# Performance work log

Measured on AMD Instinct MI355X. Metric: run time of the kernel, lower is better.

The kernel has to match this reference:

```python
import jax, jax.numpy as jnp
import numpy as np

GAMMA = 0.00390625  # 1/256


def setup_inputs() -> dict:
    key = jax.random.key(0)
    ks = jax.random.split(key, 8)
    B, F, S = 65536, 256, 1024
    return {
        "x": jax.random.normal(ks[0], (B, F), dtype=jnp.float32),
        "sv": jax.random.normal(ks[1], (S, F), dtype=jnp.float32),
        "W1": jax.random.normal(ks[2], (S, S), dtype=jnp.float32) * (1.0 / np.sqrt(S)),
        "b1": jax.random.normal(ks[3], (S,), dtype=jnp.float32) * 0.01,
        "W2": jax.random.normal(ks[4], (S, S), dtype=jnp.float32) * (1.0 / np.sqrt(S)),
        "b2": jax.random.normal(ks[5], (S,), dtype=jnp.float32) * 0.01,
        "Wh": jax.random.normal(ks[6], (2, S), dtype=jnp.float32) * (1.0 / np.sqrt(S)),
        "bh": jax.random.normal(ks[7], (2,), dtype=jnp.float32) * 0.01,
    }


def reference(x, sv, W1, b1, W2, b2, Wh, bh):
    # RBF kernel features: k[b, s] = exp(-gamma * ||x_b - sv_s||^2)
    # Expand squared distance to avoid a (B, S, F) intermediate.
    x2 = jnp.sum(x * x, axis=-1, keepdims=True)          # (B, 1)
    s2 = jnp.sum(sv * sv, axis=-1)[None, :]              # (1, S)
    d2 = x2 + s2 - 2.0 * jnp.einsum("bf,sf->bs", x, sv)  # (B, S)
    k = jnp.exp(-GAMMA * d2)                              # (B, S)
    # MLP classifier: depth=2 hidden ReLU layers + 2-logit head
    h = jax.nn.relu(jnp.einsum("bs,os->bo", k, W1) + b1)
    h = jax.nn.relu(jnp.einsum("bs,os->bo", h, W2) + b2)
    return jnp.einsum("bs,os->bo", h, Wh) + bh           # (B, 2)
```

## Files before the change

kernel.cpp:

```cpp
#include <hip/hip_runtime.h>

typedef _Float16 f16x8 __attribute__((ext_vector_type(8)));
typedef _Float16 f16x4 __attribute__((ext_vector_type(4)));
typedef float    f32x4 __attribute__((ext_vector_type(4)));

#define GAMMA_F 0.00390625f

__global__ __launch_bounds__(256) void prep_rows_kernel(
    const float* __restrict__ src, _Float16* __restrict__ dst,
    float* __restrict__ sq, int nrows)
{
    int lane = threadIdx.x & 63, w = threadIdx.x >> 6;
    int row = blockIdx.x * 4 + w;
    if (row >= nrows) return;
    float4 v = ((const float4*)(src + (size_t)row * 256))[lane];
    f16x4 h;
    h[0] = (_Float16)v.x; h[1] = (_Float16)v.y;
    h[2] = (_Float16)v.z; h[3] = (_Float16)v.w;
    *((f16x4*)(dst + (size_t)row * 256) + lane) = h;
    float ss = v.x*v.x + v.y*v.y + v.z*v.z + v.w*v.w;
#pragma unroll
    for (int off = 32; off; off >>= 1) ss += __shfl_down(ss, off);
    if (lane == 0) sq[row] = ss;
}

__global__ __launch_bounds__(256) void cvt_kernel(
    const float* __restrict__ src, _Float16* __restrict__ dst, int n4)
{
    int i = blockIdx.x * 256 + threadIdx.x;
    if (i < n4) {
        float4 v = ((const float4*)src)[i];
        f16x4 h;
        h[0] = (_Float16)v.x; h[1] = (_Float16)v.y;
        h[2] = (_Float16)v.z; h[3] = (_Float16)v.w;
        ((f16x4*)dst)[i] = h;
    }
}

#define SBAR()   __builtin_amdgcn_s_barrier()
#define RFENCE() asm volatile("" ::: "memory")

#define GLDA(gptr, uoff)                                                       \
    asm volatile("s_mov_b32 m0, %1\n\t"                                        \
                 "global_load_lds_dwordx4 %0, off\n\t"                         \
                 "s_mov_b32 m0, -1"                                            \
                 :: "v"((const void*)(gptr)), "s"(uoff))

#define UOF(x) __builtin_amdgcn_readfirstlane((x) + wb)

#define STA(s, h) do {                                                         \
    GLDA(aP##h##0, UOF((s)*32768 + (h)*16384));                                \
    GLDA(aP##h##1, UOF((s)*32768 + (h)*16384 + 8192));                         \
} while (0)
#define STB(s, h) do {                                                         \
    GLDA(bP##h##0, UOF(65536 + (s)*32768 + (h)*16384));                        \
    GLDA(bP##h##1, UOF(65536 + (s)*32768 + (h)*16384 + 8192));                 \
} while (0)
#define ADV_A() do { aP00+=64; aP01+=64; aP10+=64; aP11+=64; } while (0)
#define ADV_B() do { bP00+=64; bP01+=64; bP10+=64; bP11+=64; } while (0)

#define RD_A0(s, mh) do { _Pragma("unroll") for (int mi = 0; mi < 4; ++mi)     \
    a0f[mi] = *(const f16x8*)(ldsb + aO0 + (s)*32768 + (mh)*8192 + mi*2048);   \
} while (0)
#define RD_A1(s, mh) do { _Pragma("unroll") for (int mi = 0; mi < 4; ++mi)     \
    a1f[mi] = *(const f16x8*)(ldsb + aO1 + (s)*32768 + (mh)*8192 + mi*2048);   \
} while (0)
#define RD_B0A(s, nh) do { _Pragma("unroll") for (int nb = 0; nb < 2; ++nb)    \
    bA0[nb] = *(const f16x8*)(ldsb + bO0 + (s)*32768 + (nh)*4096 + nb*2048);   \
} while (0)
#define RD_B1A(s, nh) do { _Pragma("unroll") for (int nb = 0; nb < 2; ++nb)    \
    bA1[nb] = *(const f16x8*)(ldsb + bO1 + (s)*32768 + (nh)*4096 + nb*2048);   \
} while (0)
#define RD_B0B(s, nh) do { _Pragma("unroll") for (int nb = 0; nb < 2; ++nb)    \
    bB0[nb] = *(const f16x8*)(ldsb + bO0 + (s)*32768 + (nh)*4096 + nb*2048);   \
} while (0)
#define RD_B1B(s, nh) do { _Pragma("unroll") for (int nb = 0; nb < 2; ++nb)    \
    bB1[nb] = *(const f16x8*)(ldsb + bO1 + (s)*32768 + (nh)*4096 + nb*2048);   \
} while (0)

#define MFMA8(af, bf, mh, nh) do {                                             \
    _Pragma("unroll") for (int mi = 0; mi < 4; ++mi)                           \
    _Pragma("unroll") for (int nb = 0; nb < 2; ++nb)                           \
        acc[(mh)*4+mi][(nh)*2+nb] = __builtin_amdgcn_mfma_f32_16x16x32_f16(    \
            af[mi], bf[nb], acc[(mh)*4+mi][(nh)*2+nb], 0, 0, 0);               \
} while (0)

#define MFMA32(mh) do {                                                        \
    __builtin_amdgcn_s_setprio(1);                                             \
    MFMA8(a0f, bA0, mh, 0); MFMA8(a1f, bA1, mh, 0);                            \
    MFMA8(a0f, bB0, mh, 1); MFMA8(a1f, bB1, mh, 1);                            \
    __builtin_amdgcn_s_setprio(0);                                             \
} while (0)

template <int MODE, int K>
__global__ __launch_bounds__(512, 1) void gemm256_kernel(
    const _Float16* __restrict__ A, const _Float16* __restrict__ B,
    _Float16* __restrict__ C, const float* __restrict__ e0,
    const float* __restrict__ e1)
{
    constexpr int KT = K / 64;
    constexpr int NITER = KT / 2;
    __shared__ f16x8 lds[8192];
    char* ldsb = (char*)lds;

    const int t    = threadIdx.x;
    const int lane = t & 63, w = t >> 6;
    const int wb   = w << 10;
    const int wr   = w >> 2, wc = w & 3;
    const int lrow = lane & 15, kq = lane >> 4;

    int poison = 0;
    asm volatile("" : "+v"(poison));
    if (poison) lds[0] = f16x8{};

    int bid  = blockIdx.x;
    int cpx  = (int)(gridDim.x >> 3);
    int lbid = (bid & 7) * cpx + (bid >> 3);
    int bm   = lbid >> 2, bn = lbid & 3;
    int rowA0 = bm * 256, rowB0 = bn * 256;

    const int aO0 = ((wr*128 + lrow)*8 + ( kq      ^ (lrow & 7))) * 16;
    const int aO1 = ((wr*128 + lrow)*8 + ((4 + kq) ^ (lrow & 7))) * 16;
    const int bO0 = 65536 + ((wc*64 + lrow)*8 + ( kq      ^ (lrow & 7))) * 16;
    const int bO1 = 65536 + ((wc*64 + lrow)*8 + ((4 + kq) ^ (lrow & 7))) * 16;

    const int prow = t >> 3;
    const int cg   = (t & 7) ^ (prow & 7);
    const _Float16* aP00 = A + (size_t)(rowA0 + prow      ) * K + cg * 8;
    const _Float16* aP01 = aP00 + (size_t) 64 * K;
    const _Float16* aP10 = aP00 + (size_t)128 * K;
    const _Float16* aP11 = aP00 + (size_t)192 * K;
    const _Float16* bP00 = B + (size_t)(rowB0 + prow      ) * K + cg * 8;
    const _Float16* bP01 = bP00 + (size_t) 64 * K;
    const _Float16* bP10 = bP00 + (size_t)128 * K;
    const _Float16* bP11 = bP00 + (size_t)192 * K;

    f32x4 acc[8][4];
#pragma unroll
    for (int i = 0; i < 8; ++i)
#pragma unroll
        for (int j = 0; j < 4; ++j) acc[i][j] = (f32x4){0.f, 0.f, 0.f, 0.f};

    f16x8 a0f[4], a1f[4], bA0[2], bA1[2], bB0[2], bB1[2];

    STA(0,0); STA(0,1); STB(0,0); STB(0,1); ADV_A(); ADV_B();
    STA(1,0); STA(1,1); STB(1,0); STB(1,1); ADV_A(); ADV_B();
    asm volatile("s_waitcnt vmcnt(8)" ::: "memory");
    SBAR();

    for (int j = 0; j < NITER; ++j) {
        const bool last = (j == NITER - 1);

        RFENCE();
        RD_A0(0, 0); RD_B0A(0, 0); RD_B0B(0, 1);
        if (j > 0) { STA(1, 0); STA(1, 1); ADV_A(); }
        SBAR();
        RD_A1(0, 0); RD_B1A(0, 0); RD_B1B(0, 1);
        MFMA32(0);
        RFENCE();
        RD_A0(0, 1);
        if (!last) {
            STB(0, 0); STB(0, 1); ADV_B();
            asm volatile("s_waitcnt vmcnt(4)" ::: "memory");
        } else {
            asm volatile("s_waitcnt vmcnt(0)" ::: "memory");
        }
        SBAR();
        RD_A1(0, 1);
        MFMA32(1);
        RFENCE();
        RD_A0(1, 0); RD_B0A(1, 0); RD_B0B(1, 1);
        if (!last) { STA(0, 0); STA(0, 1); ADV_A(); }
        SBAR();
        RD_A1(1, 0); RD_B1A(1, 0); RD_B1B(1, 1);
        MFMA32(0);
        RFENCE();
        RD_A0(1, 1);
        if (!last) {
            STB(1, 0); STB(1, 1); ADV_B();
            asm volatile("s_waitcnt vmcnt(4)" ::: "memory");
        }
        SBAR();
        RD_A1(1, 1);
        MFMA32(1);
    }

    int gr0 = rowA0 + wr * 128;
    int gc0 = rowB0 + wc * 64;
    float ecol[4];
#pragma unroll
    for (int ni = 0; ni < 4; ++ni)
        ecol[ni] = (MODE == 0) ? e1[gc0 + ni * 16 + lrow]
                               : e0[gc0 + ni * 16 + lrow];
#pragma unroll
    for (int mi = 0; mi < 8; ++mi) {
#pragma unroll
        for (int jj = 0; jj < 4; ++jj) {
            int row = gr0 + mi * 16 + kq * 4 + jj;
            float xr = (MODE == 0) ? e0[row] : 0.f;
            size_t base = (size_t)row * 1024 + gc0 + lrow;
#pragma unroll
            for (int ni = 0; ni < 4; ++ni) {
                float v = acc[mi][ni][jj];
                if (MODE == 0) {
                    v = __expf(-GAMMA_F * (xr + ecol[ni] - 2.f * v));
                } else {
                    v += ecol[ni];
                    v = fmaxf(v, 0.f);
                }
                C[base + (size_t)ni * 16] = (_Float16)v;
            }
        }
    }
}

__global__ __launch_bounds__(256) void head_kernel(
    const _Float16* __restrict__ h2, const float* __restrict__ Wh,
    const float* __restrict__ bh, float* __restrict__ out)
{
    int lane = threadIdx.x & 63, w = threadIdx.x >> 6;
    int row = blockIdx.x * 4 + w;
    const _Float16* hp = h2 + (size_t)row * 1024;
    float s0 = 0.f, s1 = 0.f;
#pragma unroll
    for (int i = 0; i < 2; ++i) {
        int base = (i * 64 + lane) * 8;
        f16x8 hv = *(const f16x8*)(hp + base);
#pragma unroll
        for (int j = 0; j < 8; ++j) {
            float hj = (float)hv[j];
            s0 = fmaf(hj, Wh[base + j], s0);
            s1 = fmaf(hj, Wh[1024 + base + j], s1);
        }
    }
#pragma unroll
    for (int off = 32; off; off >>= 1) {
        s0 += __shfl_down(s0, off);
        s1 += __shfl_down(s1, off);
    }
    if (lane == 0) {
        out[(size_t)row * 2 + 0] = s0 + bh[0];
        out[(size_t)row * 2 + 1] = s1 + bh[1];
    }
}

extern "C" void kernel_launch(void* const* d_in, const int* in_sizes, int n_in,
                              void* d_out, int out_size, void* d_ws, size_t ws_size,
                              hipStream_t stream)
{
    const float* x  = (const float*)d_in[0];
    const float* sv = (const float*)d_in[1];
    const float* W1 = (const float*)d_in[2];
    const float* b1 = (const float*)d_in[3];
    const float* W2 = (const float*)d_in[4];
    const float* b2 = (const float*)d_in[5];
    const float* Wh = (const float*)d_in[6];
    const float* bh = (const float*)d_in[7];
    float* out = (float*)d_out;
    char* ws = (char*)d_ws;

    constexpr size_t OFF_SV = 0;
    constexpr size_t OFF_W1 = OFF_SV + 524288;
    constexpr size_t OFF_W2 = OFF_W1 + 2097152;
    constexpr size_t OFF_S2 = OFF_W2 + 2097152;
    constexpr size_t PERSIST = OFF_S2 + 4096;

    _Float16* svf = (_Float16*)(ws + OFF_SV);
    _Float16* w1f = (_Float16*)(ws + OFF_W1);
    _Float16* w2f = (_Float16*)(ws + OFF_W2);
    float*    s2v = (float*)(ws + OFF_S2);

    int Bc = 65536;
    while (Bc > 256 && PERSIST + (size_t)Bc * 4100ULL > ws_size) Bc >>= 1;

    char* chunk_base = ws + PERSIST;
    _Float16* kb  = (_Float16*)chunk_base;
    _Float16* h1b = (_Float16*)(chunk_base + (size_t)Bc * 2048);
    _Float16* xf  = h1b;
    float*    x2v = (float*)(chunk_base + (size_t)Bc * 4096);

    prep_rows_kernel<<<1024 / 4, 256, 0, stream>>>(sv, svf, s2v, 1024);
    cvt_kernel<<<1024, 256, 0, stream>>>(W1, w1f, 262144);
    cvt_kernel<<<1024, 256, 0, stream>>>(W2, w2f, 262144);

    int nchunks = 65536 / Bc;
    int ggrid   = (Bc / 256) * 4;
    for (int c = 0; c < nchunks; ++c) {
        const float* xc = x + (size_t)c * Bc * 256;
        prep_rows_kernel<<<Bc / 4, 256, 0, stream>>>(xc, xf, x2v, Bc);
        gemm256_kernel<0, 256><<<ggrid, 512, 0, stream>>>(xf, svf, kb, x2v, s2v);
        gemm256_kernel<1, 1024><<<ggrid, 512, 0, stream>>>(kb, w1f, h1b, b1, nullptr);
        gemm256_kernel<1, 1024><<<ggrid, 512, 0, stream>>>(h1b, w2f, kb, b2, nullptr);
        head_kernel<<<Bc / 4, 256, 0, stream>>>(kb, Wh, bh, out + (size_t)c * Bc * 2);
    }
}
```

Baseline: 372.7 us.

## Simplify GEMM main loop to one-barrier-per-tile double-buffered schedule

Replaces the hand-interleaved half-tile ping-pong schedule with a plain double-buffered loop. Each phase now waits for all outstanding global-to-LDS loads and hits one barrier, then reads every A/B fragment for the tile into registers. It then issues the next tile's loads into the other buffer and runs all 64 MFMAs. This removes several barriers and partial vmcnt waits per tile. In exchange it holds many more fragment registers and uses a full vmcnt(0) wait, which may expose memory latency that the finer interleaving used to hide.

```diff
diff --git a/kernel.cpp b/kernel.cpp
--- a/kernel.cpp
+++ b/kernel.cpp
@@ -38,7 +38,6 @@
 }
 
 #define SBAR()   __builtin_amdgcn_s_barrier()
-#define RFENCE() asm volatile("" ::: "memory")
 
 #define GLDA(gptr, uoff)                                                       \
     asm volatile("s_mov_b32 m0, %1\n\t"                                        \
@@ -48,48 +47,52 @@
 
 #define UOF(x) __builtin_amdgcn_readfirstlane((x) + wb)
 
-#define STA(s, h) do {                                                         \
-    GLDA(aP##h##0, UOF((s)*32768 + (h)*16384));                                \
-    GLDA(aP##h##1, UOF((s)*32768 + (h)*16384 + 8192));                         \
-} while (0)
-#define STB(s, h) do {                                                         \
-    GLDA(bP##h##0, UOF(65536 + (s)*32768 + (h)*16384));                        \
-    GLDA(bP##h##1, UOF(65536 + (s)*32768 + (h)*16384 + 8192));                 \
+#define STAGE_A(so) do {                                                       \
+    GLDA(aP00, UOF((so)*32768));                                               \
+    GLDA(aP01, UOF((so)*32768 + 8192));                                        \
+    GLDA(aP10, UOF((so)*32768 + 16384));                                       \
+    GLDA(aP11, UOF((so)*32768 + 24576));                                       \
+} while (0)
+#define STAGE_B(so) do {                                                       \
+    GLDA(bP00, UOF(65536 + (so)*32768));                                       \
+    GLDA(bP01, UOF(65536 + (so)*32768 + 8192));                                \
+    GLDA(bP10, UOF(65536 + (so)*32768 + 16384));                               \
+    GLDA(bP11, UOF(65536 + (so)*32768 + 24576));                               \
 } while (0)
 #define ADV_A() do { aP00+=64; aP01+=64; aP10+=64; aP11+=64; } while (0)
 #define ADV_B() do { bP00+=64; bP01+=64; bP10+=64; bP11+=64; } while (0)
 
-#define RD_A0(s, mh) do { _Pragma("unroll") for (int mi = 0; mi < 4; ++mi)     \
-    a0f[mi] = *(const f16x8*)(ldsb + aO0 + (s)*32768 + (mh)*8192 + mi*2048);   \
-} while (0)
-#define RD_A1(s, mh) do { _Pragma("unroll") for (int mi = 0; mi < 4; ++mi)     \
-    a1f[mi] = *(const f16x8*)(ldsb + aO1 + (s)*32768 + (mh)*8192 + mi*2048);   \
-} while (0)
-#define RD_B0A(s, nh) do { _Pragma("unroll") for (int nb = 0; nb < 2; ++nb)    \
-    bA0[nb] = *(const f16x8*)(ldsb + bO0 + (s)*32768 + (nh)*4096 + nb*2048);   \
-} while (0)
-#define RD_B1A(s, nh) do { _Pragma("unroll") for (int nb = 0; nb < 2; ++nb)    \
-    bA1[nb] = *(const f16x8*)(ldsb + bO1 + (s)*32768 + (nh)*4096 + nb*2048);   \
-} while (0)
-#define RD_B0B(s, nh) do { _Pragma("unroll") for (int nb = 0; nb < 2; ++nb)    \
-    bB0[nb] = *(const f16x8*)(ldsb + bO0 + (s)*32768 + (nh)*4096 + nb*2048);   \
-} while (0)
-#define RD_B1B(s, nh) do { _Pragma("unroll") for (int nb = 0; nb < 2; ++nb)    \
-    bB1[nb] = *(const f16x8*)(ldsb + bO1 + (s)*32768 + (nh)*4096 + nb*2048);   \
-} while (0)
-
-#define MFMA8(af, bf, mh, nh) do {                                             \
+#define RD_ALL(s) do {                                                         \
+    _Pragma("unroll") for (int mh = 0; mh < 2; ++mh)                           \
+    _Pragma("unroll") for (int mi = 0; mi < 4; ++mi) {                         \
+        af[0][mh*4+mi] = *(const f16x8*)(ldsb + aO0 + (s)*32768 + mh*8192 + mi*2048); \
+        af[1][mh*4+mi] = *(const f16x8*)(ldsb + aO1 + (s)*32768 + mh*8192 + mi*2048); \
+    }                                                                          \
+    _Pragma("unroll") for (int nh = 0; nh < 2; ++nh)                           \
+    _Pragma("unroll") for (int nb = 0; nb < 2; ++nb) {                         \
+        bf[0][nh*2+nb] = *(const f16x8*)(ldsb + bO0 + (s)*32768 + nh*4096 + nb*2048); \
+        bf[1][nh*2+nb] = *(const f16x8*)(ldsb + bO1 + (s)*32768 + nh*4096 + nb*2048); \
+    }                                                                          \
+} while (0)
+
+#define MFMA64() do {                                                          \
+    __builtin_amdgcn_s_setprio(1);                                             \
+    _Pragma("unroll") for (int ks = 0; ks < 2; ++ks)                           \
+    _Pragma("unroll") for (int mh = 0; mh < 2; ++mh)                           \
     _Pragma("unroll") for (int mi = 0; mi < 4; ++mi)                           \
+    _Pragma("unroll") for (int nh = 0; nh < 2; ++nh)                           \
     _Pragma("unroll") for (int nb = 0; nb < 2; ++nb)                           \
-        acc[(mh)*4+mi][(nh)*2+nb] = __builtin_amdgcn_mfma_f32_16x16x32_f16(    \
-            af[mi], bf[nb], acc[(mh)*4+mi][(nh)*2+nb], 0, 0, 0);               \
-} while (0)
-
-#define MFMA32(mh) do {                                                        \
-    __builtin_amdgcn_s_setprio(1);                                             \
-    MFMA8(a0f, bA0, mh, 0); MFMA8(a1f, bA1, mh, 0);                            \
-    MFMA8(a0f, bB0, mh, 1); MFMA8(a1f, bB1, mh, 1);                            \
+        acc[mh*4+mi][nh*2+nb] = __builtin_amdgcn_mfma_f32_16x16x32_f16(        \
+            af[ks][mh*4+mi], bf[ks][nh*2+nb], acc[mh*4+mi][nh*2+nb], 0,0,0);   \
     __builtin_amdgcn_s_setprio(0);                                             \
+} while (0)
+
+#define PHASE(s, do_stage) do {                                                \
+    asm volatile("s_waitcnt vmcnt(0)" ::: "memory");                           \
+    SBAR();                                                                    \
+    RD_ALL(s);                                                                 \
+    if (do_stage) { STAGE_A(1-(s)); STAGE_B(1-(s)); ADV_A(); ADV_B(); }        \
+    MFMA64();                                                                  \
 } while (0)
 
 template <int MODE, int K>
@@ -99,7 +102,6 @@
     const float* __restrict__ e1)
 {
     constexpr int KT = K / 64;
-    constexpr int NITER = KT / 2;
     __shared__ f16x8 lds[8192];
     char* ldsb = (char*)lds;
 
@@ -141,48 +143,13 @@
 #pragma unroll
         for (int j = 0; j < 4; ++j) acc[i][j] = (f32x4){0.f, 0.f, 0.f, 0.f};
 
-    f16x8 a0f[4], a1f[4], bA0[2], bA1[2], bB0[2], bB1[2];
-
-    STA(0,0); STA(0,1); STB(0,0); STB(0,1); ADV_A(); ADV_B();
-    STA(1,0); STA(1,1); STB(1,0); STB(1,1); ADV_A(); ADV_B();
-    asm volatile("s_waitcnt vmcnt(8)" ::: "memory");
-    SBAR();
-
-    for (int j = 0; j < NITER; ++j) {
-        const bool last = (j == NITER - 1);
-
-        RFENCE();
-        RD_A0(0, 0); RD_B0A(0, 0); RD_B0B(0, 1);
-        if (j > 0) { STA(1, 0); STA(1, 1); ADV_A(); }
-        SBAR();
-        RD_A1(0, 0); RD_B1A(0, 0); RD_B1B(0, 1);
-        MFMA32(0);
-        RFENCE();
-        RD_A0(0, 1);
-        if (!last) {
-            STB(0, 0); STB(0, 1); ADV_B();
-            asm volatile("s_waitcnt vmcnt(4)" ::: "memory");
-        } else {
-            asm volatile("s_waitcnt vmcnt(0)" ::: "memory");
-        }
-        SBAR();
-        RD_A1(0, 1);
-        MFMA32(1);
-        RFENCE();
-        RD_A0(1, 0); RD_B0A(1, 0); RD_B0B(1, 1);
-        if (!last) { STA(0, 0); STA(0, 1); ADV_A(); }
-        SBAR();
-        RD_A1(1, 0); RD_B1A(1, 0); RD_B1B(1, 1);
-        MFMA32(0);
-        RFENCE();
-        RD_A0(1, 1);
-        if (!last) {
-            STB(1, 0); STB(1, 1); ADV_B();
-            asm volatile("s_waitcnt vmcnt(4)" ::: "memory");
-        }
-        SBAR();
-        RD_A1(1, 1);
-        MFMA32(1);
+    f16x8 af[2][8], bf[2][4];
+
+    STAGE_A(0); STAGE_B(0); ADV_A(); ADV_B();
+
+    for (int j = 0; j < KT / 2; ++j) {
+        PHASE(0, 1);
+        PHASE(1, j < KT / 2 - 1);
     }
 
     int gr0 = rowA0 + wr * 128;
```

Result: slower. 447.4 us (+20.0%).
